# Optimization experiments

Hardware: AMD Instinct MI355X
Metric: run time of the kernel (lower is better)

Reference implementation:

```python
import jax, jax.numpy as jnp
import numpy as np

FS = 30.0        # sampling rate
N = 512          # input_size (time samples)
BIN_RES = 0.001  # frequency resolution
C, S = 32, 256   # channel / spatial dims of x
F_LO, F_HI = 0.66, 2.5


def _chirp_consts():
    """Deterministic CZT constants, matching the torch module's construction."""
    freq_zoom = np.arange(F_LO, F_HI, BIN_RES, dtype=np.float64)
    M = len(freq_zoom)  # 1840
    dt = 1.0 / FS  # (t[-1]-t[0])/(N-1) == 1/fs for t = arange(N)/fs
    df = (freq_zoom[-1] - freq_zoom[0]) / (M - 1)
    # A (phase ramp) diagonal values: 2*pi*f0*(-k)*dt, k = 0..N-1
    k = np.arange(N)
    a_vals = 2.0 * np.pi * freq_zoom[0] * (-k) * dt
    a_cos = np.cos(a_vals).astype(np.float32)
    a_sin = np.sin(a_vals).astype(np.float32)
    # W chirp matrix: -2*pi*df*k*n*dt, k in [0,M), n in [0,N)
    kv = np.arange(M)[:, None]
    nv = np.arange(N)[None, :]
    w_vals = -2.0 * np.pi * df * kv * nv * dt
    W_real = np.cos(w_vals).astype(np.float32)
    W_imag = np.sin(w_vals).astype(np.float32)
    return W_real, W_imag, a_cos, a_sin


def setup_inputs() -> dict:
    key = jax.random.key(0)
    x = jax.random.normal(key, (N, C, S), dtype=jnp.float32)
    W_real, W_imag, a_cos, a_sin = _chirp_consts()
    return {
        "x": x,
        "W_real": jnp.asarray(W_real),
        "W_imag": jnp.asarray(W_imag),
        "a_cos": jnp.asarray(a_cos),
        "a_sin": jnp.asarray(a_sin),
    }


def reference(x, W_real, W_imag, a_cos, a_sin):
    # A is diagonal -> diag matmul == per-row broadcast scaling (same math).
    Ax_real = a_cos[:, None, None] * x  # [N, C, S]
    Ax_imag = a_sin[:, None, None] * x  # [N, C, S]
    Ax = jnp.concatenate([Ax_real, Ax_imag], axis=0)  # [2N, C, S]
    # Block chirp matrix [[Wr, -Wi], [Wi, Wr]] -> [2M, 2N]
    W = jnp.concatenate(
        [
            jnp.concatenate([W_real, -W_imag], axis=1),
            jnp.concatenate([W_imag, W_real], axis=1),
        ],
        axis=0,
    )
    W = jnp.clip(W, -1.0, 1.0)  # Hardtanh (no-op on cos/sin, kept for fidelity)
    X = jnp.einsum("ji,ics->jcs", W, Ax)  # [2M, C, S]
    return W, X
```

## Files before the change

kernel.cpp:

```cpp
#include <hip/hip_runtime.h>
#include <hip/hip_bf16.h>
#include <stdint.h>

#define MM   1840
#define M2   3680
#define NN   512
#define K2   1024
#define CS   8192
#define MPAD 3712

#define WPREP_BLOCKS (MPAD / 2)
#define XT_NB        (CS / 32)
#define XT_KB        (NN / 64)

typedef __bf16 bf16x8 __attribute__((ext_vector_type(8)));
typedef float  floatx4 __attribute__((ext_vector_type(4)));

__global__ __launch_bounds__(256) void czt_prep(const float* __restrict__ Wr,
                                                const float* __restrict__ Wi,
                                                const float* __restrict__ ac,
                                                const float* __restrict__ as_,
                                                const float* __restrict__ x,
                                                float* __restrict__ Wout,
                                                __hip_bfloat16* __restrict__ Abf,
                                                __hip_bfloat16* __restrict__ Bxt) {
    __shared__ float tile[64 * 33];
    const int b   = blockIdx.x;
    const int tid = threadIdx.x;

    if (b < WPREP_BLOCKS) {
        const int j = b * 2 + (tid >> 7);
        const int k = (tid & 127) * 4;

        union { __hip_bfloat16 h[4]; uint2 u; } p;
        if (j < M2) {
            const int jj = (j < MM) ? j : j - MM;
            const float4 wr = *(const float4*)&Wr[(size_t)jj * NN + k];
            const float4 wi = *(const float4*)&Wi[(size_t)jj * NN + k];
            const float4 c  = *(const float4*)&ac[k];
            const float4 s  = *(const float4*)&as_[k];
            float4 f, g;
            float a0, a1, a2, a3;
            if (j < MM) {
                f = wr;
                g.x = -wi.x; g.y = -wi.y; g.z = -wi.z; g.w = -wi.w;
                a0 = wr.x * c.x - wi.x * s.x;
                a1 = wr.y * c.y - wi.y * s.y;
                a2 = wr.z * c.z - wi.z * s.z;
                a3 = wr.w * c.w - wi.w * s.w;
            } else {
                f = wi;
                g = wr;
                a0 = wi.x * c.x + wr.x * s.x;
                a1 = wi.y * c.y + wr.y * s.y;
                a2 = wi.z * c.z + wr.z * s.z;
                a3 = wi.w * c.w + wr.w * s.w;
            }
            f.x = fminf(1.f, fmaxf(-1.f, f.x)); f.y = fminf(1.f, fmaxf(-1.f, f.y));
            f.z = fminf(1.f, fmaxf(-1.f, f.z)); f.w = fminf(1.f, fmaxf(-1.f, f.w));
            g.x = fminf(1.f, fmaxf(-1.f, g.x)); g.y = fminf(1.f, fmaxf(-1.f, g.y));
            g.z = fminf(1.f, fmaxf(-1.f, g.z)); g.w = fminf(1.f, fmaxf(-1.f, g.w));
            *(float4*)&Wout[(size_t)j * K2 + k]      = f;
            *(float4*)&Wout[(size_t)j * K2 + NN + k] = g;
            p.h[0] = __float2bfloat16(a0);
            p.h[1] = __float2bfloat16(a1);
            p.h[2] = __float2bfloat16(a2);
            p.h[3] = __float2bfloat16(a3);
        } else {
            p.h[0] = p.h[1] = p.h[2] = p.h[3] = __float2bfloat16(0.0f);
        }
        *(uint2*)&Abf[(size_t)j * NN + k] = p.u;
    } else {
        const int tb = b - WPREP_BLOCKS;
        const int n0 = (tb & (XT_NB - 1)) * 32;
        const int k0 = (tb >> 8) * 64;

        const int row = tid >> 2;
        const int c8  = (tid & 3) * 8;
        const float* src = &x[(size_t)(k0 + row) * CS + n0 + c8];
        const float4 v0 = *(const float4*)src;
        const float4 v1 = *(const float4*)(src + 4);
        float* tr = &tile[row * 33 + c8];
        tr[0] = v0.x; tr[1] = v0.y; tr[2] = v0.z; tr[3] = v0.w;
        tr[4] = v1.x; tr[5] = v1.y; tr[6] = v1.z; tr[7] = v1.w;
        __syncthreads();

        const int oc = tid & 7;
        const int nr = tid >> 3;
        union { __hip_bfloat16 h[8]; uint4 u; } q;
#pragma unroll
        for (int jj = 0; jj < 8; ++jj)
            q.h[jj] = __float2bfloat16(tile[(oc * 8 + jj) * 33 + nr]);
        *(uint4*)&Bxt[(size_t)(n0 + nr) * NN + k0 + oc * 8] = q.u;
    }
}

__device__ __forceinline__ void gload_lds16(const void* g, void* l) {
    __builtin_amdgcn_global_load_lds(
        (const __attribute__((address_space(1))) uint32_t*)g,
        (__attribute__((address_space(3))) uint32_t*)l,
        16, 0, 0);
}

__global__ __launch_bounds__(256) void czt_gemm(const __hip_bfloat16* __restrict__ Abf,
                                                const __hip_bfloat16* __restrict__ Bxt,
                                                float* __restrict__ Xout) {
    __shared__ __hip_bfloat16 As[128 * 64];
    __shared__ __hip_bfloat16 Bs[128 * 64];

    const int tid  = threadIdx.x;
    const int lane = tid & 63;
    const int w    = tid >> 6;
    const int quad = lane >> 4;
    const int r16  = lane & 15;

    const int mtile = blockIdx.y * 128;
    const int ntile = blockIdx.x * 128;
    const int wm = (w >> 1) * 64;
    const int wn = (w & 1) * 64;

    const int rstage = w * 32 + (lane >> 3);
    const int cstage = (lane & 7) * 8;
    const __hip_bfloat16* Ag = Abf + (size_t)(mtile + rstage) * NN + cstage;
    const __hip_bfloat16* Bg = Bxt + (size_t)(ntile + rstage) * NN + cstage;

    floatx4 acc[4][4] = {};

#pragma unroll 1
    for (int kt = 0; kt < NN / 64; ++kt) {
        __syncthreads();
#pragma unroll
        for (int t = 0; t < 4; ++t) {
            gload_lds16(Ag + (size_t)(t * 8) * NN + kt * 64, &As[(w * 32 + t * 8) * 64]);
            gload_lds16(Bg + (size_t)(t * 8) * NN + kt * 64, &Bs[(w * 32 + t * 8) * 64]);
        }
        __syncthreads();

#pragma unroll
        for (int ks = 0; ks < 2; ++ks) {
            bf16x8 af[4], bfr[4];
#pragma unroll
            for (int i = 0; i < 4; ++i) {
                af[i]  = *(const bf16x8*)&As[(wm + i * 16 + r16) * 64 + ks * 32 + quad * 8];
                bfr[i] = *(const bf16x8*)&Bs[(wn + i * 16 + r16) * 64 + ks * 32 + quad * 8];
            }
#pragma unroll
            for (int i = 0; i < 4; ++i)
#pragma unroll
                for (int jn = 0; jn < 4; ++jn)
                    acc[i][jn] = __builtin_amdgcn_mfma_f32_16x16x32_bf16(
                        af[i], bfr[jn], acc[i][jn], 0, 0, 0);
        }
    }

#pragma unroll
    for (int i = 0; i < 4; ++i) {
        const int rbase = mtile + wm + i * 16 + quad * 4;
#pragma unroll
        for (int rr = 0; rr < 4; ++rr) {
            const int rg = rbase + rr;
            if (rg < M2) {
#pragma unroll
                for (int jn = 0; jn < 4; ++jn) {
                    const int cg = ntile + wn + jn * 16 + r16;
                    Xout[(size_t)rg * CS + cg] = acc[i][jn][rr];
                }
            }
        }
    }
}

extern "C" void kernel_launch(void* const* d_in, const int* in_sizes, int n_in,
                              void* d_out, int out_size, void* d_ws, size_t ws_size,
                              hipStream_t stream) {
    const float* x   = (const float*)d_in[0];
    const float* Wr  = (const float*)d_in[1];
    const float* Wi  = (const float*)d_in[2];
    const float* ac  = (const float*)d_in[3];
    const float* as_ = (const float*)d_in[4];

    float* Wout = (float*)d_out;
    float* Xout = (float*)d_out + (size_t)M2 * K2;

    __hip_bfloat16* Abf = (__hip_bfloat16*)d_ws;
    __hip_bfloat16* Bxt = (__hip_bfloat16*)((char*)d_ws + (size_t)MPAD * NN * 2);

    czt_prep<<<dim3(WPREP_BLOCKS + XT_NB * XT_KB), dim3(256), 0, stream>>>(
        Wr, Wi, ac, as_, x, Wout, Abf, Bxt);
    czt_gemm<<<dim3(CS / 128, MPAD / 128), dim3(256), 0, stream>>>(Abf, Bxt, Xout);
}
```

Before: 194.7 us.

## Remap GEMM blocks per XCD for L2 reuse and use nontemporal stores

Flattens the GEMM grid to 1D and remaps block IDs so that each of the 8 XCDs owns a contiguous range of N tiles and iterates over all M tiles, so its B tiles can be reused in that XCD's L2. The large fp32 outputs (W copy and X) are written, and x is read, with nontemporal hints to reduce cache pollution. The K loop is also fully unrolled. The remap relies on round-robin block-to-XCD dispatch, and full unrolling may raise register pressure.

```diff
diff --git a/kernel.cpp b/kernel.cpp
--- a/kernel.cpp
+++ b/kernel.cpp
@@ -8,6 +8,9 @@
 #define K2   1024
 #define CS   8192
 #define MPAD 3712
+
+#define NB_M 29
+#define NB_N 64
 
 #define WPREP_BLOCKS (MPAD / 2)
 #define XT_NB        (CS / 32)
@@ -35,37 +38,32 @@
         union { __hip_bfloat16 h[4]; uint2 u; } p;
         if (j < M2) {
             const int jj = (j < MM) ? j : j - MM;
-            const float4 wr = *(const float4*)&Wr[(size_t)jj * NN + k];
-            const float4 wi = *(const float4*)&Wi[(size_t)jj * NN + k];
-            const float4 c  = *(const float4*)&ac[k];
-            const float4 s  = *(const float4*)&as_[k];
-            float4 f, g;
-            float a0, a1, a2, a3;
+            const floatx4 wr = *(const floatx4*)&Wr[(size_t)jj * NN + k];
+            const floatx4 wi = *(const floatx4*)&Wi[(size_t)jj * NN + k];
+            const floatx4 c  = *(const floatx4*)&ac[k];
+            const floatx4 s  = *(const floatx4*)&as_[k];
+            floatx4 f, g;
+            floatx4 a;
             if (j < MM) {
                 f = wr;
-                g.x = -wi.x; g.y = -wi.y; g.z = -wi.z; g.w = -wi.w;
-                a0 = wr.x * c.x - wi.x * s.x;
-                a1 = wr.y * c.y - wi.y * s.y;
-                a2 = wr.z * c.z - wi.z * s.z;
-                a3 = wr.w * c.w - wi.w * s.w;
+                g = -wi;
+                a = wr * c - wi * s;
             } else {
                 f = wi;
                 g = wr;
-                a0 = wi.x * c.x + wr.x * s.x;
-                a1 = wi.y * c.y + wr.y * s.y;
-                a2 = wi.z * c.z + wr.z * s.z;
-                a3 = wi.w * c.w + wr.w * s.w;
+                a = wi * c + wr * s;
             }
-            f.x = fminf(1.f, fmaxf(-1.f, f.x)); f.y = fminf(1.f, fmaxf(-1.f, f.y));
-            f.z = fminf(1.f, fmaxf(-1.f, f.z)); f.w = fminf(1.f, fmaxf(-1.f, f.w));
-            g.x = fminf(1.f, fmaxf(-1.f, g.x)); g.y = fminf(1.f, fmaxf(-1.f, g.y));
-            g.z = fminf(1.f, fmaxf(-1.f, g.z)); g.w = fminf(1.f, fmaxf(-1.f, g.w));
-            *(float4*)&Wout[(size_t)j * K2 + k]      = f;
-            *(float4*)&Wout[(size_t)j * K2 + NN + k] = g;
-            p.h[0] = __float2bfloat16(a0);
-            p.h[1] = __float2bfloat16(a1);
-            p.h[2] = __float2bfloat16(a2);
-            p.h[3] = __float2bfloat16(a3);
+#pragma unroll
+            for (int e = 0; e < 4; ++e) {
+                f[e] = fminf(1.f, fmaxf(-1.f, f[e]));
+                g[e] = fminf(1.f, fmaxf(-1.f, g[e]));
+            }
+            __builtin_nontemporal_store(f, (floatx4*)&Wout[(size_t)j * K2 + k]);
+            __builtin_nontemporal_store(g, (floatx4*)&Wout[(size_t)j * K2 + NN + k]);
+            p.h[0] = __float2bfloat16(a[0]);
+            p.h[1] = __float2bfloat16(a[1]);
+            p.h[2] = __float2bfloat16(a[2]);
+            p.h[3] = __float2bfloat16(a[3]);
         } else {
             p.h[0] = p.h[1] = p.h[2] = p.h[3] = __float2bfloat16(0.0f);
         }
@@ -77,12 +75,12 @@
 
         const int row = tid >> 2;
         const int c8  = (tid & 3) * 8;
-        const float* src = &x[(size_t)(k0 + row) * CS + n0 + c8];
-        const float4 v0 = *(const float4*)src;
-        const float4 v1 = *(const float4*)(src + 4);
+        const floatx4* src = (const floatx4*)&x[(size_t)(k0 + row) * CS + n0 + c8];
+        const floatx4 v0 = __builtin_nontemporal_load(src);
+        const floatx4 v1 = __builtin_nontemporal_load(src + 1);
         float* tr = &tile[row * 33 + c8];
-        tr[0] = v0.x; tr[1] = v0.y; tr[2] = v0.z; tr[3] = v0.w;
-        tr[4] = v1.x; tr[5] = v1.y; tr[6] = v1.z; tr[7] = v1.w;
+        tr[0] = v0[0]; tr[1] = v0[1]; tr[2] = v0[2]; tr[3] = v0[3];
+        tr[4] = v1[0]; tr[5] = v1[1]; tr[6] = v1[2]; tr[7] = v1[3];
         __syncthreads();
 
         const int oc = tid & 7;
@@ -114,8 +112,14 @@
     const int quad = lane >> 4;
     const int r16  = lane & 15;
 
-    const int mtile = blockIdx.y * 128;
-    const int ntile = blockIdx.x * 128;
+    const int b    = blockIdx.x;
+    const int xcd  = b & 7;
+    const int i    = b >> 3;
+    const int mb   = i % NB_M;
+    const int nl   = i / NB_M;
+    const int mtile = mb * 128;
+    const int ntile = (xcd * 8 + nl) * 128;
+
     const int wm = (w >> 1) * 64;
     const int wn = (w & 1) * 64;
 
@@ -126,7 +130,7 @@
 
     floatx4 acc[4][4] = {};
 
-#pragma unroll 1
+#pragma unroll
     for (int kt = 0; kt < NN / 64; ++kt) {
         __syncthreads();
 #pragma unroll
@@ -140,22 +144,22 @@
         for (int ks = 0; ks < 2; ++ks) {
             bf16x8 af[4], bfr[4];
 #pragma unroll
-            for (int i = 0; i < 4; ++i) {
-                af[i]  = *(const bf16x8*)&As[(wm + i * 16 + r16) * 64 + ks * 32 + quad * 8];
-                bfr[i] = *(const bf16x8*)&Bs[(wn + i * 16 + r16) * 64 + ks * 32 + quad * 8];
+            for (int i2 = 0; i2 < 4; ++i2) {
+                af[i2]  = *(const bf16x8*)&As[(wm + i2 * 16 + r16) * 64 + ks * 32 + quad * 8];
+                bfr[i2] = *(const bf16x8*)&Bs[(wn + i2 * 16 + r16) * 64 + ks * 32 + quad * 8];
             }
 #pragma unroll
-            for (int i = 0; i < 4; ++i)
+            for (int i2 = 0; i2 < 4; ++i2)
 #pragma unroll
                 for (int jn = 0; jn < 4; ++jn)
-                    acc[i][jn] = __builtin_amdgcn_mfma_f32_16x16x32_bf16(
-                        af[i], bfr[jn], acc[i][jn], 0, 0, 0);
+                    acc[i2][jn] = __builtin_amdgcn_mfma_f32_16x16x32_bf16(
+                        af[i2], bfr[jn], acc[i2][jn], 0, 0, 0);
         }
     }
 
 #pragma unroll
-    for (int i = 0; i < 4; ++i) {
-        const int rbase = mtile + wm + i * 16 + quad * 4;
+    for (int i2 = 0; i2 < 4; ++i2) {
+        const int rbase = mtile + wm + i2 * 16 + quad * 4;
 #pragma unroll
         for (int rr = 0; rr < 4; ++rr) {
             const int rg = rbase + rr;
@@ -163,7 +167,8 @@
 #pragma unroll
                 for (int jn = 0; jn < 4; ++jn) {
                     const int cg = ntile + wn + jn * 16 + r16;
-                    Xout[(size_t)rg * CS + cg] = acc[i][jn][rr];
+                    __builtin_nontemporal_store(acc[i2][jn][rr],
+                                                &Xout[(size_t)rg * CS + cg]);
                 }
             }
         }
@@ -187,5 +192,5 @@
 
     czt_prep<<<dim3(WPREP_BLOCKS + XT_NB * XT_KB), dim3(256), 0, stream>>>(
         Wr, Wi, ac, as_, x, Wout, Abf, Bxt);
-    czt_gemm<<<dim3(CS / 128, MPAD / 128), dim3(256), 0, stream>>>(Abf, Bxt, Xout);
+    czt_gemm<<<dim3(NB_M * NB_N), dim3(256), 0, stream>>>(Abf, Bxt, Xout);
 }
```

After: 196.2 us. Within noise of the previous version (+0.7%).
